# Optimization experiments

Hardware: AMD Instinct MI355X
Metric: run time of the kernel (lower is better)

Reference implementation:

```python
import jax, jax.numpy as jnp
import numpy as np

B, T, E, DK, H = 8, 2048, 1024, 64, 16  # dk*num_heads == embedding_dim


def setup_inputs() -> dict:
    key = jax.random.key(0)
    kx, kq, kk, kv, kl = jax.random.split(key, 5)
    x = jax.random.normal(kx, (B, T, E), dtype=jnp.float32)
    # zero-pad a random tail of each sequence so the data-derived padding mask
    # in the forward (length = count of nonzero energy[b,0,:]) is exercised
    lengths = jax.random.randint(kl, (B,), T // 2, T + 1)
    valid = (jnp.arange(T)[None, :, None] < lengths[:, None, None]).astype(jnp.float32)
    x = x * valid
    scale = 0.02
    Wq = jax.random.normal(kq, (E, DK * H), dtype=jnp.float32) * scale
    Wk = jax.random.normal(kk, (E, DK * H), dtype=jnp.float32) * scale
    Wv = jax.random.normal(kv, (E, DK * H), dtype=jnp.float32) * scale
    return {"x": x, "Wq": Wq, "Wk": Wk, "Wv": Wv}


def reference(x, Wq, Wk, Wv):
    # Q,K,V: [B, T, DK*H] (heads are fused, matching the source's bmm math)
    Q = jnp.einsum('bte,ed->btd', x, Wq)
    K = jnp.einsum('bte,ed->btd', x, Wk)
    V = jnp.einsum('bte,ed->btd', x, Wv)
    energy = jnp.einsum('btd,bsd->bts', Q, K)  # [B, T, T]
    # vectorized version of the per-batch loop: length from nonzeros of row 0,
    # then mask all key columns >= length with -inf
    lengths = jnp.sum(energy[:, 0, :] != 0, axis=-1)              # [B]
    col_mask = jnp.arange(T)[None, :] >= lengths[:, None]          # [B, T]
    energy = jnp.where(col_mask[:, None, :], -jnp.inf, energy)
    score = jax.nn.softmax(energy / jnp.sqrt(jnp.float32(DK)), axis=-1)
    return jnp.einsum('bts,bsd->btd', score, V)  # [B, T, DK*H]
```

## Files before the change

### kernel.cpp

```cpp
#include <hip/hip_runtime.h>
#include <hip/hip_bf16.h>


typedef unsigned short u16;
typedef __bf16 bf16x8 __attribute__((ext_vector_type(8)));
typedef float f32x4 __attribute__((ext_vector_type(4)));
typedef unsigned short us8 __attribute__((ext_vector_type(8)));

__device__ __forceinline__ u16 f2bf(float f) {
    union { float f; unsigned u; } x; x.f = f;
    unsigned r = x.u + 0x7FFFu + ((x.u >> 16) & 1u);
    return (u16)(r >> 16);
}
__device__ __forceinline__ u16 f2h(float f) {
    union { _Float16 h; u16 u; } c; c.h = (_Float16)f;
    return c.u;
}
__device__ __forceinline__ float h2f(u16 b) {
    union { u16 u; _Float16 h; } c; c.u = b;
    return (float)c.h;
}

__device__ __forceinline__ void gload_lds16(const void* g, void* l) {
    __builtin_amdgcn_global_load_lds(
        (const __attribute__((address_space(1))) unsigned*)g,
        (__attribute__((address_space(3))) unsigned*)l, 16, 0, 0);
}

__global__ void cast_x(const float* __restrict__ x, u16* __restrict__ o) {
    int i = blockIdx.x * 256 + threadIdx.x;
    float4 v = ((const float4*)x)[i];
    ushort4 u;
    u.x = f2bf(v.x); u.y = f2bf(v.y); u.z = f2bf(v.z); u.w = f2bf(v.w);
    ((ushort4*)o)[i] = u;
}

__global__ void transpose_cast_w(const float* __restrict__ Wq,
                                 const float* __restrict__ Wk,
                                 const float* __restrict__ Wv,
                                 u16* __restrict__ WT) {
    __shared__ float tile[32][33];
    const float* W = (blockIdx.z == 0) ? Wq : (blockIdx.z == 1) ? Wk : Wv;
    u16* T = WT + (size_t)blockIdx.z * 1048576;
    int n0 = blockIdx.x * 32, e0 = blockIdx.y * 32;
    int tx = threadIdx.x, ty = threadIdx.y;
#pragma unroll
    for (int j = 0; j < 4; ++j) {
        int e = ty + j * 8;
        tile[e][tx] = W[(size_t)(e0 + e) * 1024 + (n0 + tx)];
    }
    __syncthreads();
#pragma unroll
    for (int j = 0; j < 4; ++j) {
        int n = ty + j * 8;
        T[(size_t)(n0 + n) * 1024 + (e0 + tx)] = f2bf(tile[tx][n]);
    }
}

__global__ void calc_lengths(const float* __restrict__ x, int* __restrict__ len) {
    int b = blockIdx.x, tid = threadIdx.x;
    int cnt = 0;
    for (int t = tid; t < 2048; t += 256) {
        float4 v = *(const float4*)(x + ((size_t)b * 2048 + t) * 1024);
        cnt += (v.x != 0.f || v.y != 0.f || v.z != 0.f || v.w != 0.f) ? 1 : 0;
    }
#pragma unroll
    for (int off = 32; off; off >>= 1) cnt += __shfl_xor(cnt, off);
    __shared__ int red[4];
    int wid = tid >> 6, lane = tid & 63;
    if (!lane) red[wid] = cnt;
    __syncthreads();
    if (tid == 0) len[b] = red[0] + red[1] + red[2] + red[3];
}

template <int MODE>
__global__ __launch_bounds__(256, 3)
void gemm_bt(const u16* __restrict__ A, int lda, size_t sA,
             const u16* __restrict__ B, int ldb, size_t sB,
             void* __restrict__ Cv, void* __restrict__ Cv2,
             int ldc, size_t sC, int Kdim, const int* __restrict__ lenp) {
    __shared__ u16 As[128 * 32];
    __shared__ u16 Bs[128 * 32];
    const int tid = threadIdx.x;
    const int bz  = blockIdx.z;
    A += (size_t)bz * sA;
    B += (size_t)bz * sB;
    const size_t bm = (size_t)blockIdx.x * 128, bn = (size_t)blockIdx.y * 128;

    bool skip_loop = false;
    int kEnd = Kdim;
    if (MODE == 3) {
        int lenz = lenp[bm >> 11];
        skip_loop = ((int)(bm & 2047) >= lenz);
    } else if (MODE == 4) {
        int lenz = lenp[bz];
        if ((int)bn >= lenz) return;
    } else if (MODE == 5) {
        int lenz = lenp[bz];
        int r32 = (lenz + 31) & ~31;
        kEnd = r32 < Kdim ? r32 : Kdim;
    }

    const int r0 = tid >> 2;
    const int c0 = (tid & 3) * 8;
    const u16* a0 = A + (bm + r0) * (size_t)lda + c0;
    const u16* a1 = a0 + 64 * (size_t)lda;
    const u16* b0 = B + (bn + r0) * (size_t)ldb + c0;
    const u16* b1 = b0 + 64 * (size_t)ldb;
    u16* As0 = &As[tid * 8];
    u16* As1 = &As[(tid + 256) * 8];
    u16* Bs0 = &Bs[tid * 8];
    u16* Bs1 = &Bs[(tid + 256) * 8];

    const int wid = tid >> 6, lane = tid & 63;
    const int wrow = (wid >> 1) * 64, wcol = (wid & 1) * 64;
    const int q = lane >> 4, r = lane & 15;

    f32x4 acc[4][4] = {};

    if (!skip_loop) {
        for (int k0 = 0; k0 < kEnd; k0 += 32) {
            gload_lds16(a0 + k0, As0);
            gload_lds16(a1 + k0, As1);
            gload_lds16(b0 + k0, Bs0);
            gload_lds16(b1 + k0, Bs1);
            __syncthreads();
            bf16x8 af[4], bfr[4];
#pragma unroll
            for (int mt = 0; mt < 4; ++mt)
                af[mt] = *(const bf16x8*)&As[(wrow + mt * 16 + r) * 32 + q * 8];
#pragma unroll
            for (int nt = 0; nt < 4; ++nt)
                bfr[nt] = *(const bf16x8*)&Bs[(wcol + nt * 16 + r) * 32 + q * 8];
#pragma unroll
            for (int mt = 0; mt < 4; ++mt)
#pragma unroll
                for (int nt = 0; nt < 4; ++nt)
                    acc[mt][nt] = __builtin_amdgcn_mfma_f32_16x16x32_bf16(
                        af[mt], bfr[nt], acc[mt][nt], 0, 0, 0);
            __syncthreads();
        }
    }

    if (MODE == 5) {
        float* C = (float*)Cv + (size_t)bz * sC;
#pragma unroll
        for (int mt = 0; mt < 4; ++mt) {
            size_t row = bm + wrow + mt * 16 + q * 4;
#pragma unroll
            for (int nt = 0; nt < 4; ++nt) {
                size_t col = bn + wcol + nt * 16 + r;
#pragma unroll
                for (int i = 0; i < 4; ++i)
                    C[(row + i) * (size_t)ldc + col] = acc[mt][nt][i];
            }
        }
    } else if (MODE == 4) {
        u16* C = (u16*)Cv + (size_t)bz * sC;
#pragma unroll
        for (int mt = 0; mt < 4; ++mt) {
            size_t row = bm + wrow + mt * 16 + q * 4;
#pragma unroll
            for (int nt = 0; nt < 4; ++nt) {
                size_t col = bn + wcol + nt * 16 + r;
#pragma unroll
                for (int i = 0; i < 4; ++i)
                    C[(row + i) * (size_t)ldc + col] = f2h(acc[mt][nt][i]);
            }
        }
    } else {
        int region = blockIdx.y >> 3;
        if (region < 2) {
            u16* C = (u16*)Cv + (size_t)region * 16777216;
            size_t cb = bn - (size_t)region * 1024;
#pragma unroll
            for (int mt = 0; mt < 4; ++mt) {
                size_t row = bm + wrow + mt * 16 + q * 4;
#pragma unroll
                for (int nt = 0; nt < 4; ++nt) {
                    size_t col = cb + wcol + nt * 16 + r;
#pragma unroll
                    for (int i = 0; i < 4; ++i)
                        C[(row + i) * 1024 + col] = f2bf(acc[mt][nt][i]);
                }
            }
        } else {
            u16* Cb = (u16*)Cv2 + (bm >> 11) * (size_t)(1024 * 2048)
                      + (bn - 2048) * 2048 + (bm & 2047)
                      + (size_t)(wcol + r) * 2048 + (wrow + q * 4);
#pragma unroll
            for (int nt = 0; nt < 4; ++nt) {
#pragma unroll
                for (int mt = 0; mt < 4; ++mt) {
                    ushort4 o;
                    o.x = f2bf(acc[mt][nt][0]);
                    o.y = f2bf(acc[mt][nt][1]);
                    o.z = f2bf(acc[mt][nt][2]);
                    o.w = f2bf(acc[mt][nt][3]);
                    *(ushort4*)(Cb + (size_t)(nt * 16) * 2048 + mt * 16) = o;
                }
            }
        }
    }
}

__global__ void softmax_rows_w(u16* __restrict__ E, const int* __restrict__ lengths) {
    int row  = blockIdx.x * 4 + (threadIdx.x >> 6);
    int lane = threadIdx.x & 63;
    int len  = lengths[row >> 11];
    u16* e = E + (size_t)row * 2048;

    float vals[32];
#pragma unroll
    for (int j = 0; j < 4; ++j) {
        us8 v = ((const us8*)e)[j * 64 + lane];
#pragma unroll
        for (int w = 0; w < 8; ++w) vals[j * 8 + w] = h2f(v[w]);
    }

    float m = -3.4e38f;
#pragma unroll
    for (int j = 0; j < 4; ++j) {
        int base = (j * 64 + lane) * 8;
#pragma unroll
        for (int w = 0; w < 8; ++w)
            if (base + w < len) m = fmaxf(m, vals[j * 8 + w]);
    }
#pragma unroll
    for (int off = 32; off; off >>= 1) m = fmaxf(m, __shfl_xor(m, off));

    const float C = 0.18033688011112042f;
    float p[32]; float s = 0.f;
#pragma unroll
    for (int j = 0; j < 4; ++j) {
        int base = (j * 64 + lane) * 8;
#pragma unroll
        for (int w = 0; w < 8; ++w) {
            float v = (base + w < len) ? exp2f((vals[j * 8 + w] - m) * C) : 0.f;
            p[j * 8 + w] = v;
            s += v;
        }
    }
#pragma unroll
    for (int off = 32; off; off >>= 1) s += __shfl_xor(s, off);
    float rinv = 1.0f / s;

#pragma unroll
    for (int j = 0; j < 4; ++j) {
        us8 o;
#pragma unroll
        for (int w = 0; w < 8; ++w) o[w] = f2bf(p[j * 8 + w] * rinv);
        ((us8*)e)[j * 64 + lane] = o;
    }
}

extern "C" void kernel_launch(void* const* d_in, const int* in_sizes, int n_in,
                              void* d_out, int out_size, void* d_ws, size_t ws_size,
                              hipStream_t stream) {
    const float* x  = (const float*)d_in[0];
    const float* Wq = (const float*)d_in[1];
    const float* Wk = (const float*)d_in[2];
    const float* Wv = (const float*)d_in[3];
    float* out = (float*)d_out;
    char* ws = (char*)d_ws;

    const size_t SB  = 2097152;
    const size_t SBe = 4194304;

    if (ws_size < 140509440ULL) return;
    int* lengths = (int*)ws;
    u16* x16 = (u16*)(ws + 256);
    u16* WT  = (u16*)(ws + 33554688);
    u16* VT  = (u16*)(ws + 39846144);
    u16* E   = (u16*)(ws + 73400576);
    u16* Qb  = (u16*)d_out;
    u16* Kb  = Qb + 16777216;

    cast_x<<<dim3(16384), dim3(256), 0, stream>>>(x, x16);
    transpose_cast_w<<<dim3(32, 32, 3), dim3(32, 8), 0, stream>>>(Wq, Wk, Wv, WT);
    calc_lengths<<<dim3(8), dim3(256), 0, stream>>>(x, lengths);

    gemm_bt<3><<<dim3(128, 24, 1), 256, 0, stream>>>(x16, 1024, 0, WT, 1024, 0,
                                                     Qb, VT, 0, 0, 1024, lengths);

    gemm_bt<4><<<dim3(16, 16, 8), 256, 0, stream>>>(Qb, 1024, SB, Kb, 1024, SB,
                                                    E, nullptr, 2048, SBe, 1024, lengths);

    softmax_rows_w<<<dim3(4096), dim3(256), 0, stream>>>(E, lengths);

    gemm_bt<5><<<dim3(16, 8, 8), 256, 0, stream>>>(E, 2048, SBe, VT, 2048, SB,
                                                   out, nullptr, 1024, SB, 2048, lengths);
}
```

Before: 415.6 us.

## Rewrite bf16 GEMM as 256x256 double-buffered swizzled tile with phased MFMA scheduling

The GEMM kernel moves from a single-buffered 128x128x32 tile with 256 threads to a 256x256x64 tile with 512 threads. It double-buffers the async global-to-LDS loads with XOR-swizzled LDS layout, and interleaves LDS fragment loads with MFMA quads using sched barriers and setprio. The goal is to hide load latency, cut LDS bank conflicts and raise data reuse per block. The QK^T mode now also skips the K loop for query rows past the sequence length. The trade-offs are a large LDS footprint of 128KB per block, and far fewer blocks for the smaller GEMMs, which can leave CUs underused, especially for the PV GEMM that launches only 256 blocks.

```diff
diff --git a/kernel.cpp b/kernel.cpp
--- a/kernel.cpp
+++ b/kernel.cpp
@@ -73,131 +73,187 @@
     if (tid == 0) len[b] = red[0] + red[1] + red[2] + red[3];
 }
 
+
+#define PHASE_SEP do { __builtin_amdgcn_sched_barrier(0); \
+                       __builtin_amdgcn_s_barrier(); \
+                       __builtin_amdgcn_sched_barrier(0); } while (0)
+
+#define STAGE_T(KT, BUF) do { \
+  _Pragma("unroll") for (int j_ = 0; j_ < 4; ++j_) \
+      gload_lds16(A + offA[j_] + (size_t)(KT) * 64, &As[BUF][ldsC[j_]]); \
+  _Pragma("unroll") for (int j_ = 0; j_ < 4; ++j_) \
+      gload_lds16(B + offB[j_] + (size_t)(KT) * 64, &Bs[BUF][ldsC[j_]]); \
+} while (0)
+
+#define LD_A4(AF, BUF, MH) do { \
+  _Pragma("unroll") for (int s_ = 0; s_ < 2; ++s_) \
+  _Pragma("unroll") for (int mt_ = 0; mt_ < 4; ++mt_) { \
+    int row_ = arow0 + (MH) * 64 + mt_ * 16 + r; \
+    AF[s_][mt_] = *(const bf16x8*)&As[BUF][row_ * 64 + (((q + s_ * 4) ^ (row_ & 7)) * 8)]; \
+  } \
+} while (0)
+
+#define LD_B2(BF, BUF, NH) do { \
+  _Pragma("unroll") for (int s_ = 0; s_ < 2; ++s_) \
+  _Pragma("unroll") for (int nt_ = 0; nt_ < 2; ++nt_) { \
+    int row_ = brow0 + (NH) * 32 + nt_ * 16 + r; \
+    BF[s_][nt_] = *(const bf16x8*)&Bs[BUF][row_ * 64 + (((q + s_ * 4) ^ (row_ & 7)) * 8)]; \
+  } \
+} while (0)
+
+#define MFMA_QUAD(AF, BF, MH, NH) do { \
+  _Pragma("unroll") for (int s_ = 0; s_ < 2; ++s_) \
+  _Pragma("unroll") for (int mt_ = 0; mt_ < 4; ++mt_) \
+  _Pragma("unroll") for (int nt_ = 0; nt_ < 2; ++nt_) \
+    acc[(MH) * 4 + mt_][(NH) * 2 + nt_] = __builtin_amdgcn_mfma_f32_16x16x32_bf16( \
+        AF[s_][mt_], BF[s_][nt_], acc[(MH) * 4 + mt_][(NH) * 2 + nt_], 0, 0, 0); \
+} while (0)
+
 template <int MODE>
-__global__ __launch_bounds__(256, 3)
+__global__ __launch_bounds__(512, 2)
 void gemm_bt(const u16* __restrict__ A, int lda, size_t sA,
              const u16* __restrict__ B, int ldb, size_t sB,
              void* __restrict__ Cv, void* __restrict__ Cv2,
              int ldc, size_t sC, int Kdim, const int* __restrict__ lenp) {
-    __shared__ u16 As[128 * 32];
-    __shared__ u16 Bs[128 * 32];
+    __shared__ u16 As[2][256 * 64];
+    __shared__ u16 Bs[2][256 * 64];
     const int tid = threadIdx.x;
     const int bz  = blockIdx.z;
     A += (size_t)bz * sA;
     B += (size_t)bz * sB;
-    const size_t bm = (size_t)blockIdx.x * 128, bn = (size_t)blockIdx.y * 128;
-
-    bool skip_loop = false;
+    const size_t bm = (size_t)blockIdx.x * 256, bn = (size_t)blockIdx.y * 256;
+
+    bool skip = false;
     int kEnd = Kdim;
     if (MODE == 3) {
         int lenz = lenp[bm >> 11];
-        skip_loop = ((int)(bm & 2047) >= lenz);
+        skip = ((int)(bm & 2047) >= lenz);
     } else if (MODE == 4) {
         int lenz = lenp[bz];
         if ((int)bn >= lenz) return;
+        skip = ((int)bm >= lenz);
     } else if (MODE == 5) {
         int lenz = lenp[bz];
-        int r32 = (lenz + 31) & ~31;
-        kEnd = r32 < Kdim ? r32 : Kdim;
-    }
-
-    const int r0 = tid >> 2;
-    const int c0 = (tid & 3) * 8;
-    const u16* a0 = A + (bm + r0) * (size_t)lda + c0;
-    const u16* a1 = a0 + 64 * (size_t)lda;
-    const u16* b0 = B + (bn + r0) * (size_t)ldb + c0;
-    const u16* b1 = b0 + 64 * (size_t)ldb;
-    u16* As0 = &As[tid * 8];
-    u16* As1 = &As[(tid + 256) * 8];
-    u16* Bs0 = &Bs[tid * 8];
-    u16* Bs1 = &Bs[(tid + 256) * 8];
+        int r64 = (lenz + 63) & ~63;
+        kEnd = r64 < Kdim ? r64 : Kdim;
+    }
 
     const int wid = tid >> 6, lane = tid & 63;
-    const int wrow = (wid >> 1) * 64, wcol = (wid & 1) * 64;
+    const int wm = wid >> 2, wn = wid & 3;
     const int q = lane >> 4, r = lane & 15;
-
-    f32x4 acc[4][4] = {};
-
-    if (!skip_loop) {
-        for (int k0 = 0; k0 < kEnd; k0 += 32) {
-            gload_lds16(a0 + k0, As0);
-            gload_lds16(a1 + k0, As1);
-            gload_lds16(b0 + k0, Bs0);
-            gload_lds16(b1 + k0, Bs1);
-            __syncthreads();
-            bf16x8 af[4], bfr[4];
-#pragma unroll
-            for (int mt = 0; mt < 4; ++mt)
-                af[mt] = *(const bf16x8*)&As[(wrow + mt * 16 + r) * 32 + q * 8];
-#pragma unroll
-            for (int nt = 0; nt < 4; ++nt)
-                bfr[nt] = *(const bf16x8*)&Bs[(wcol + nt * 16 + r) * 32 + q * 8];
-#pragma unroll
-            for (int mt = 0; mt < 4; ++mt)
-#pragma unroll
-                for (int nt = 0; nt < 4; ++nt)
-                    acc[mt][nt] = __builtin_amdgcn_mfma_f32_16x16x32_bf16(
-                        af[mt], bfr[nt], acc[mt][nt], 0, 0, 0);
-            __syncthreads();
+    const int arow0 = wm * 128, brow0 = wn * 64;
+
+    size_t offA[4], offB[4]; int ldsC[4];
+#pragma unroll
+    for (int j = 0; j < 4; ++j) {
+        int c = j * 512 + tid;
+        int row = c >> 3;
+        int c16 = (c & 7) ^ (row & 7);
+        offA[j] = (size_t)(bm + row) * lda + c16 * 8;
+        offB[j] = (size_t)(bn + row) * ldb + c16 * 8;
+        ldsC[j] = c * 8;
+    }
+
+    f32x4 acc[8][4] = {};
+
+    if (!skip) {
+        const int NT = kEnd >> 6;
+        STAGE_T(0, 0);
+        STAGE_T(1, 1);
+        asm volatile("s_waitcnt vmcnt(8)" ::: "memory");
+        PHASE_SEP;
+        for (int t = 0; t < NT; ++t) {
+            const int p = t & 1;
+            bf16x8 a[2][4], b0[2][2], b1[2][2];
+            LD_A4(a, p, 0);
+            LD_B2(b0, p, 0);
+            PHASE_SEP;
+            __builtin_amdgcn_s_setprio(1);
+            MFMA_QUAD(a, b0, 0, 0);
+            __builtin_amdgcn_s_setprio(0);
+            PHASE_SEP;
+            LD_B2(b1, p, 1);
+            PHASE_SEP;
+            __builtin_amdgcn_s_setprio(1);
+            MFMA_QUAD(a, b1, 0, 1);
+            __builtin_amdgcn_s_setprio(0);
+            PHASE_SEP;
+            LD_A4(a, p, 1);
+            PHASE_SEP;
+            __builtin_amdgcn_s_setprio(1);
+            MFMA_QUAD(a, b1, 1, 1);
+            __builtin_amdgcn_s_setprio(0);
+            PHASE_SEP;
+            if (t + 2 < NT) STAGE_T(t + 2, p);
+            PHASE_SEP;
+            __builtin_amdgcn_s_setprio(1);
+            MFMA_QUAD(a, b0, 1, 0);
+            __builtin_amdgcn_s_setprio(0);
+            __builtin_amdgcn_sched_barrier(0);
+            if (t + 2 < NT)      asm volatile("s_waitcnt vmcnt(8)" ::: "memory");
+            else if (t + 1 < NT) asm volatile("s_waitcnt vmcnt(0)" ::: "memory");
+            __builtin_amdgcn_s_barrier();
+            __builtin_amdgcn_sched_barrier(0);
         }
     }
 
     if (MODE == 5) {
         float* C = (float*)Cv + (size_t)bz * sC;
 #pragma unroll
-        for (int mt = 0; mt < 4; ++mt) {
-            size_t row = bm + wrow + mt * 16 + q * 4;
-#pragma unroll
-            for (int nt = 0; nt < 4; ++nt) {
-                size_t col = bn + wcol + nt * 16 + r;
+        for (int am = 0; am < 8; ++am) {
+            size_t row = bm + arow0 + (am >> 2) * 64 + (am & 3) * 16 + q * 4;
+#pragma unroll
+            for (int an = 0; an < 4; ++an) {
+                size_t col = bn + brow0 + (an >> 1) * 32 + (an & 1) * 16 + r;
 #pragma unroll
                 for (int i = 0; i < 4; ++i)
-                    C[(row + i) * (size_t)ldc + col] = acc[mt][nt][i];
+                    C[(row + i) * (size_t)ldc + col] = acc[am][an][i];
             }
         }
     } else if (MODE == 4) {
         u16* C = (u16*)Cv + (size_t)bz * sC;
 #pragma unroll
-        for (int mt = 0; mt < 4; ++mt) {
-            size_t row = bm + wrow + mt * 16 + q * 4;
-#pragma unroll
-            for (int nt = 0; nt < 4; ++nt) {
-                size_t col = bn + wcol + nt * 16 + r;
+        for (int am = 0; am < 8; ++am) {
+            size_t row = bm + arow0 + (am >> 2) * 64 + (am & 3) * 16 + q * 4;
+#pragma unroll
+            for (int an = 0; an < 4; ++an) {
+                size_t col = bn + brow0 + (an >> 1) * 32 + (an & 1) * 16 + r;
 #pragma unroll
                 for (int i = 0; i < 4; ++i)
-                    C[(row + i) * (size_t)ldc + col] = f2h(acc[mt][nt][i]);
+                    C[(row + i) * (size_t)ldc + col] = f2h(acc[am][an][i]);
             }
         }
     } else {
-        int region = blockIdx.y >> 3;
+        int region = blockIdx.y >> 2;
         if (region < 2) {
             u16* C = (u16*)Cv + (size_t)region * 16777216;
             size_t cb = bn - (size_t)region * 1024;
 #pragma unroll
-            for (int mt = 0; mt < 4; ++mt) {
-                size_t row = bm + wrow + mt * 16 + q * 4;
-#pragma unroll
-                for (int nt = 0; nt < 4; ++nt) {
-                    size_t col = cb + wcol + nt * 16 + r;
+            for (int am = 0; am < 8; ++am) {
+                size_t row = bm + arow0 + (am >> 2) * 64 + (am & 3) * 16 + q * 4;
+#pragma unroll
+                for (int an = 0; an < 4; ++an) {
+                    size_t col = cb + brow0 + (an >> 1) * 32 + (an & 1) * 16 + r;
 #pragma unroll
                     for (int i = 0; i < 4; ++i)
-                        C[(row + i) * 1024 + col] = f2bf(acc[mt][nt][i]);
+                        C[(row + i) * 1024 + col] = f2bf(acc[am][an][i]);
                 }
             }
         } else {
             u16* Cb = (u16*)Cv2 + (bm >> 11) * (size_t)(1024 * 2048)
-                      + (bn - 2048) * 2048 + (bm & 2047)
-                      + (size_t)(wcol + r) * 2048 + (wrow + q * 4);
-#pragma unroll
-            for (int nt = 0; nt < 4; ++nt) {
-#pragma unroll
-                for (int mt = 0; mt < 4; ++mt) {
+                      + (bn - 2048) * 2048 + (bm & 2047);
+#pragma unroll
+            for (int an = 0; an < 4; ++an) {
+                int cI = brow0 + (an >> 1) * 32 + (an & 1) * 16 + r;
+#pragma unroll
+                for (int am = 0; am < 8; ++am) {
+                    int tI = arow0 + (am >> 2) * 64 + (am & 3) * 16 + q * 4;
                     ushort4 o;
-                    o.x = f2bf(acc[mt][nt][0]);
-                    o.y = f2bf(acc[mt][nt][1]);
-                    o.z = f2bf(acc[mt][nt][2]);
-                    o.w = f2bf(acc[mt][nt][3]);
-                    *(ushort4*)(Cb + (size_t)(nt * 16) * 2048 + mt * 16) = o;
+                    o.x = f2bf(acc[am][an][0]);
+                    o.y = f2bf(acc[am][an][1]);
+                    o.z = f2bf(acc[am][an][2]);
+                    o.w = f2bf(acc[am][an][3]);
+                    *(ushort4*)(Cb + (size_t)cI * 2048 + tI) = o;
                 }
             }
         }
@@ -280,14 +336,14 @@
     transpose_cast_w<<<dim3(32, 32, 3), dim3(32, 8), 0, stream>>>(Wq, Wk, Wv, WT);
     calc_lengths<<<dim3(8), dim3(256), 0, stream>>>(x, lengths);
 
-    gemm_bt<3><<<dim3(128, 24, 1), 256, 0, stream>>>(x16, 1024, 0, WT, 1024, 0,
-                                                     Qb, VT, 0, 0, 1024, lengths);
-
-    gemm_bt<4><<<dim3(16, 16, 8), 256, 0, stream>>>(Qb, 1024, SB, Kb, 1024, SB,
-                                                    E, nullptr, 2048, SBe, 1024, lengths);
+    gemm_bt<3><<<dim3(64, 12, 1), 512, 0, stream>>>(x16, 1024, 0, WT, 1024, 0,
+                                                    Qb, VT, 1024, 0, 1024, lengths);
+
+    gemm_bt<4><<<dim3(8, 8, 8), 512, 0, stream>>>(Qb, 1024, SB, Kb, 1024, SB,
+                                                  E, nullptr, 2048, SBe, 1024, lengths);
 
     softmax_rows_w<<<dim3(4096), dim3(256), 0, stream>>>(E, lengths);
 
-    gemm_bt<5><<<dim3(16, 8, 8), 256, 0, stream>>>(E, 2048, SBe, VT, 2048, SB,
-                                                   out, nullptr, 1024, SB, 2048, lengths);
-}
+    gemm_bt<5><<<dim3(8, 4, 8), 512, 0, stream>>>(E, 2048, SBe, VT, 2048, SB,
+                                                  out, nullptr, 1024, SB, 2048, lengths);
+}
```

After: 405.5 us. 1.02x faster.
